# Performance work log

Hardware: AMD Instinct MI355X
Metric: run time of the kernel (lower is better)

## Reference

```python
import jax, jax.numpy as jnp
import numpy as np
import math

B, L, C_IN, D, H, FACTOR = 32, 512, 32, 512, 8, 1
E = D // H
TOP_K = int(FACTOR * math.log(L))  # 6


def setup_inputs() -> dict:
    key = jax.random.key(0)
    ks = jax.random.split(key, 14)
    s = 0.02
    f = lambda k, shp: jax.random.normal(k, shp, jnp.float32) * s
    return {
        "x": jax.random.normal(ks[0], (B, L, C_IN), jnp.float32),
        "conv_w": f(ks[1], (D, C_IN)),  # Conv1d kernel_size=1 == pointwise linear
        "conv_b": f(ks[2], (D,)),
        "wq": f(ks[3], (D, D)), "bq": f(ks[4], (D,)),
        "wk": f(ks[5], (D, D)), "bk": f(ks[6], (D,)),
        "wv": f(ks[7], (D, D)), "bv": f(ks[8], (D,)),
        "wo": f(ks[9], (D, D)), "bo": f(ks[10], (D,)),
        "lin_w": f(ks[11], (1, D)), "lin_b": f(ks[12], (1,)),
    }


def _autocorrelation(q, k, v):
    # q, k, v: [B, L, H, E]; Autoformer AutoCorrelation (inference delay agg)
    qf = jnp.fft.rfft(q.transpose(0, 2, 3, 1), axis=-1)        # [B,H,E,Lf]
    kf = jnp.fft.rfft(k.transpose(0, 2, 3, 1), axis=-1)
    corr = jnp.fft.irfft(qf * jnp.conj(kf), n=L, axis=-1)       # [B,H,E,L]
    vals = v.transpose(0, 2, 3, 1)                              # [B,H,E,L]
    mean_corr = corr.mean(axis=(1, 2))                          # [B,L]
    weights, delay = jax.lax.top_k(mean_corr, TOP_K)            # [B,k]
    w = jax.nn.softmax(weights, axis=-1)                        # [B,k]
    # gather values at (t + delay) mod L  (== doubled-values trick in torch)
    idx = (jnp.arange(L)[None, None, :] + delay[:, :, None]) % L  # [B,k,L]
    patterns = jnp.take_along_axis(
        vals[:, :, :, None, :], idx[:, None, None, :, :], axis=-1)  # [B,H,E,k,L]
    agg = jnp.einsum('bhekl,bk->bhel', patterns, w)             # [B,H,E,L]
    return agg.transpose(0, 3, 1, 2)                            # [B,L,H,E]


def reference(x, conv_w, conv_b, wq, bq, wk, bk, wv, bv, wo, bo, lin_w, lin_b):
    # pointwise conv1d projection: [B,L,C_IN] -> [B,L,D]
    h = x @ conv_w.T + conv_b
    q = (h @ wq.T + bq).reshape(B, L, H, E)
    k = (h @ wk.T + bk).reshape(B, L, H, E)
    v = (h @ wv.T + bv).reshape(B, L, H, E)
    attn_out = _autocorrelation(q, k, v).reshape(B, L, D)
    new_x = attn_out @ wo.T + bo
    out = h + new_x          # residual
    last = out[:, -1:, :]    # x[:, -1:]
    y = last @ lin_w.T + lin_b  # [B,1,1]
    return y
```

## Files before the change

### kernel.cpp

```cpp
#include <hip/hip_runtime.h>
#include <hip/hip_bf16.h>

#define LL 512
#define BB 32
#define DD 512
#define CINN 32
#define TOPK 6
#define BL (BB * LL)

typedef __attribute__((ext_vector_type(8))) short bf16x8;
typedef __attribute__((ext_vector_type(4))) float f32x4;

__device__ inline float bf2f(ushort u) {
    union { uint i; float f; } c; c.i = ((uint)u) << 16; return c.f;
}
__device__ inline ushort f2bf(float f) {
    union { float f; uint i; } c; c.f = f;
    uint i = c.i;
    return (ushort)((i + 0x7FFFu + ((i >> 16) & 1u)) >> 16);
}
__device__ inline void split_bf(float v, ushort& hi, ushort& lo) {
    hi = f2bf(v);
    lo = f2bf(v - bf2f(hi));
}
__device__ inline uint pk2(ushort a, ushort b) { return (uint)a | ((uint)b << 16); }

__device__ inline bf16x8 frag_ld(const ushort* sm, int r, int s) {
    return *(const bf16x8*)(sm + r * 32 + ((s ^ ((r >> 1) & 3)) << 3));
}

__device__ inline void mfma_step(const ushort* sAh, const ushort* sAl,
                                 const ushort* sBh, const ushort* sBl,
                                 f32x4 acc[4][4], int wr, int wc, int fr, int fs) {
    bf16x8 bh[4], blo[4];
    #pragma unroll
    for (int ni = 0; ni < 4; ++ni) {
        bh[ni]  = frag_ld(sBh, wc + ni * 16 + fr, fs);
        blo[ni] = frag_ld(sBl, wc + ni * 16 + fr, fs);
    }
    #pragma unroll
    for (int mi = 0; mi < 4; ++mi) {
        const bf16x8 ah = frag_ld(sAh, wr + mi * 16 + fr, fs);
        const bf16x8 al = frag_ld(sAl, wr + mi * 16 + fr, fs);
        #pragma unroll
        for (int ni = 0; ni < 4; ++ni) {
            acc[mi][ni] = __builtin_amdgcn_mfma_f32_16x16x32_bf16(ah, bh[ni],  acc[mi][ni], 0, 0, 0);
            acc[mi][ni] = __builtin_amdgcn_mfma_f32_16x16x32_bf16(ah, blo[ni], acc[mi][ni], 0, 0, 0);
            acc[mi][ni] = __builtin_amdgcn_mfma_f32_16x16x32_bf16(al, bh[ni],  acc[mi][ni], 0, 0, 0);
        }
    }
}

__global__ __launch_bounds__(256) void prep_m(
    const float* __restrict__ wq, const float* __restrict__ wk,
    const float* __restrict__ cw,
    const float* __restrict__ lin_w, const float* __restrict__ wo,
    float* __restrict__ Mpart, float* __restrict__ upart)
{
    const int tid = threadIdx.x;
    if (blockIdx.x < 64) {
        __shared__ float cws[512][32];
        __shared__ float wqsT[512][9];
        __shared__ float wksT[512][9];
        __shared__ float aqs[8][32];
        __shared__ float aks[8][32];
        for (int i = tid; i < 4096; i += 256) {
            const int d = i >> 3, q = i & 7;
            *(float4*)&cws[d][q * 4] = *(const float4*)(cw + (long)d * 32 + q * 4);
        }
        const int e0 = blockIdx.x * 8;
        for (int i = tid; i < 4096; i += 256) {
            const int e = i >> 9, d = i & 511;
            wqsT[d][e] = wq[(long)(e0 + e) * 512 + d];
            wksT[d][e] = wk[(long)(e0 + e) * 512 + d];
        }
        __syncthreads();
        const int e_loc = tid >> 5, c = tid & 31;
        float aq = 0.f, ak = 0.f;
        #pragma unroll 4
        for (int d = 0; d < 512; ++d) {
            const float cv = cws[d][c];
            aq += wqsT[d][e_loc] * cv;
            ak += wksT[d][e_loc] * cv;
        }
        aqs[e_loc][c] = aq;
        aks[e_loc][c] = ak;
        __syncthreads();
        const int c_ = tid >> 3, cq = tid & 7;
        float m0 = 0.f, m1 = 0.f, m2 = 0.f, m3 = 0.f;
        #pragma unroll
        for (int e = 0; e < 8; ++e) {
            const float a = aqs[e][c_];
            const float4 k4 = *(const float4*)&aks[e][cq * 4];
            m0 += a * k4.x; m1 += a * k4.y; m2 += a * k4.z; m3 += a * k4.w;
        }
        *(float4*)(Mpart + (long)blockIdx.x * 1024 + c_ * 32 + cq * 4) =
            make_float4(m0, m1, m2, m3);
    } else {
        const int j = blockIdx.x - 64;
        const int n0 = j * 64;
        float u0 = 0.f, u1 = 0.f;
        for (int n = 0; n < 64; ++n) {
            const float lw = lin_w[n0 + n];
            u0 += lw * wo[(long)(n0 + n) * 512 + tid];
            u1 += lw * wo[(long)(n0 + n) * 512 + tid + 256];
        }
        upart[j * 512 + tid] = u0;
        upart[j * 512 + tid + 256] = u1;
    }
}

__global__ __launch_bounds__(256, 2) void corr_fused(
    const float* __restrict__ x,
    const float* __restrict__ Mpart, const float* __restrict__ upart,
    const float* __restrict__ wv,
    float* __restrict__ mcpart, float* __restrict__ v2part)
{
    const int tid = threadIdx.x;
    if (blockIdx.x < 512) {
        __shared__ ushort buf[16384];
        __shared__ float Ml[32][36];
        __shared__ float mcloc[LL];
        ushort* bufAh = buf;
        ushort* bufAl = buf + 4096;
        ushort* bufBh = buf + 8192;
        ushort* bufBl = buf + 12288;

        const int xcd = blockIdx.x & 7, s = blockIdx.x >> 3;
        const int b = xcd * 4 + (s >> 4);
        const int tile = s & 15;
        const int tm = tile >> 2, tn = tile & 3;

        {
            float4 ms = make_float4(0.f, 0.f, 0.f, 0.f);
            for (int p = 0; p < 64; ++p) {
                const float4 v = *(const float4*)(Mpart + (long)p * 1024 + tid * 4);
                ms.x += v.x; ms.y += v.y; ms.z += v.z; ms.w += v.w;
            }
            *(float4*)&Ml[tid >> 3][(tid & 7) * 4] = ms;
        }
        mcloc[tid] = 0.f; mcloc[tid + 256] = 0.f;

        const int r = tid >> 1;
        const int pb = (tid & 1) * 2;
        const int swz = (r >> 1) & 3;
        const float* xA = x + ((long)b * LL + tm * 128 + r) * 32;
        const float* xB = x + ((long)b * LL + tn * 128 + r) * 32;
        float xb[32];
        #pragma unroll
        for (int q = 0; q < 8; ++q)
            *(float4*)&xb[q * 4] = *(const float4*)(xB + q * 4);

        __syncthreads();

        #pragma unroll
        for (int pi = 0; pi < 2; ++pi) {
            const int p = pb + pi;
            const int sl = p ^ swz;
            const int uoff = (r * 4 + p) * 8;
            const float4 a0 = *(const float4*)(xA + sl * 8);
            const float4 a1 = *(const float4*)(xA + sl * 8 + 4);
            const float xe[8] = {a0.x, a0.y, a0.z, a0.w, a1.x, a1.y, a1.z, a1.w};
            ushort xh[8], xl[8];
            #pragma unroll
            for (int j = 0; j < 8; ++j) split_bf(xe[j], xh[j], xl[j]);
            *(uint4*)(bufAh + uoff) = make_uint4(pk2(xh[0], xh[1]), pk2(xh[2], xh[3]),
                                                 pk2(xh[4], xh[5]), pk2(xh[6], xh[7]));
            *(uint4*)(bufAl + uoff) = make_uint4(pk2(xl[0], xl[1]), pk2(xl[2], xl[3]),
                                                 pk2(xl[4], xl[5]), pk2(xl[6], xl[7]));
            float uv[8];
            #pragma unroll
            for (int j = 0; j < 8; ++j) {
                const int c = sl * 8 + j;
                float sacc = 0.f;
                #pragma unroll
                for (int q = 0; q < 8; ++q) {
                    const float4 m = *(const float4*)&Ml[c][q * 4];
                    sacc += m.x * xb[q * 4] + m.y * xb[q * 4 + 1]
                          + m.z * xb[q * 4 + 2] + m.w * xb[q * 4 + 3];
                }
                uv[j] = sacc;
            }
            ushort uh[8], ul[8];
            #pragma unroll
            for (int j = 0; j < 8; ++j) split_bf(uv[j], uh[j], ul[j]);
            *(uint4*)(bufBh + uoff) = make_uint4(pk2(uh[0], uh[1]), pk2(uh[2], uh[3]),
                                                 pk2(uh[4], uh[5]), pk2(uh[6], uh[7]));
            *(uint4*)(bufBl + uoff) = make_uint4(pk2(ul[0], ul[1]), pk2(ul[2], ul[3]),
                                                 pk2(ul[4], ul[5]), pk2(ul[6], ul[7]));
        }
        __syncthreads();

        const int wid = tid >> 6, lane = tid & 63;
        const int wr = (wid >> 1) * 64, wc = (wid & 1) * 64;
        const int fr = lane & 15, fs = lane >> 4;
        f32x4 acc[4][4] = {};
        mfma_step(bufAh, bufAl, bufBh, bufBl, acc, wr, wc, fr, fs);

        const int base = wr - wc + 128 * (tm - tn) + fs * 4 - fr;
        #pragma unroll
        for (int k = -3; k <= 3; ++k) {
            #pragma unroll
            for (int rr = 0; rr < 4; ++rr) {
                float sdg = 0.f;
                #pragma unroll
                for (int mi = 0; mi < 4; ++mi) {
                    const int ni = mi - k;
                    if (ni >= 0 && ni < 4) sdg += acc[mi][ni][rr];
                }
                atomicAdd(&mcloc[(base + 16 * k + rr) & (LL - 1)], sdg);
            }
        }
        __syncthreads();
        float* out = mcpart + ((long)b * 16 + tile) * LL;
        out[tid] = mcloc[tid];
        out[tid + 256] = mcloc[tid + 256];
    } else {
        const int j = blockIdx.x - 512;
        __shared__ float us[64];
        if (tid < 64) {
            float s = 0.f;
            #pragma unroll
            for (int i = 0; i < 8; ++i) s += upart[i * 512 + j * 64 + tid];
            us[tid] = s;
        }
        __syncthreads();
        float s0 = 0.f, s1 = 0.f;
        for (int dl = 0; dl < 64; ++dl) {
            const float ud = us[dl];
            s0 += ud * wv[(long)(j * 64 + dl) * 512 + tid];
            s1 += ud * wv[(long)(j * 64 + dl) * 512 + tid + 256];
        }
        v2part[j * 512 + tid] = s0;
        v2part[j * 512 + tid + 256] = s1;
    }
}

__global__ __launch_bounds__(256) void tail_kernel(
    const float* __restrict__ mcpart, const float* __restrict__ x,
    const float* __restrict__ upart, const float* __restrict__ v2part,
    const float* __restrict__ cw, const float* __restrict__ cb,
    const float* __restrict__ lin_w, const float* __restrict__ bv,
    const float* __restrict__ bo, const float* __restrict__ lin_b,
    float* __restrict__ out)
{
    const int b = blockIdx.x, tid = threadIdx.x;
    const int lane = tid & 63, wid = tid >> 6;
    __shared__ float v2s[512];
    __shared__ float us2[512];
    __shared__ float w3p[8][32];
    __shared__ float w4p[8][32];
    __shared__ float w3s[32];
    __shared__ float w4s[32];
    __shared__ float c2s;
    __shared__ float swv[4];
    __shared__ int   swi[4];
    __shared__ float selv[TOPK];
    __shared__ int   seli[TOPK];
    __shared__ float wts[TOPK];
    __shared__ float redc[4];

    {
        float a0 = 0.f, a1 = 0.f, b0 = 0.f, b1 = 0.f;
        #pragma unroll
        for (int i = 0; i < 8; ++i) {
            a0 += v2part[i * 512 + tid];
            a1 += v2part[i * 512 + tid + 256];
            b0 += upart[i * 512 + tid];
            b1 += upart[i * 512 + tid + 256];
        }
        v2s[tid] = a0; v2s[tid + 256] = a1;
        us2[tid] = b0; us2[tid + 256] = b1;
    }
    __syncthreads();
    {
        const int c = tid & 31, g = tid >> 5;
        float w3 = 0.f, w4 = 0.f;
        for (int dl = 0; dl < 64; ++dl) {
            const int d = g * 64 + dl;
            const float cwv = cw[(long)d * 32 + c];
            w3 += v2s[d] * cwv;
            w4 += lin_w[d] * cwv;
        }
        w3p[g][c] = w3; w4p[g][c] = w4;
    }
    __syncthreads();
    if (tid < 32) {
        float a3 = 0.f, a4 = 0.f;
        #pragma unroll
        for (int g2 = 0; g2 < 8; ++g2) { a3 += w3p[g2][tid]; a4 += w4p[g2][tid]; }
        w3s[tid] = a3; w4s[tid] = a4;
    }
    {
        float p = cb[tid] * (v2s[tid] + lin_w[tid])
                + cb[tid + 256] * (v2s[tid + 256] + lin_w[tid + 256])
                + bv[tid] * us2[tid] + bv[tid + 256] * us2[tid + 256]
                + bo[tid] * lin_w[tid] + bo[tid + 256] * lin_w[tid + 256];
        #pragma unroll
        for (int o = 32; o; o >>= 1) p += __shfl_down(p, o);
        if ((tid & 63) == 0) redc[tid >> 6] = p;
    }
    __syncthreads();
    if (tid == 0) c2s = redc[0] + redc[1] + redc[2] + redc[3] + lin_b[0];

    float v0 = 0.f, v1 = 0.f;
    #pragma unroll
    for (int j = 0; j < 16; ++j) {
        v0 += mcpart[((long)b * 16 + j) * LL + tid];
        v1 += mcpart[((long)b * 16 + j) * LL + tid + 256];
    }
    v0 *= (1.0f / DD); v1 *= (1.0f / DD);

    int live0 = 1, live1 = 1;
    for (int r = 0; r < TOPK; ++r) {
        float bvv = -1e30f; int bi = -1;
        if (live0) { bvv = v0; bi = tid; }
        if (live1 && v1 > bvv) { bvv = v1; bi = tid + 256; }
        #pragma unroll
        for (int o = 32; o; o >>= 1) {
            const float ov = __shfl_down(bvv, o);
            const int oi = __shfl_down(bi, o);
            if (ov > bvv || (ov == bvv && oi < bi)) { bvv = ov; bi = oi; }
        }
        if (lane == 0) { swv[wid] = bvv; swi[wid] = bi; }
        __syncthreads();
        if (tid == 0) {
            float fv = swv[0]; int fi = swi[0];
            #pragma unroll
            for (int w2 = 1; w2 < 4; ++w2) {
                if (swv[w2] > fv || (swv[w2] == fv && swi[w2] < fi)) { fv = swv[w2]; fi = swi[w2]; }
            }
            selv[r] = fv; seli[r] = fi;
        }
        __syncthreads();
        const int w = seli[r];
        if (w == tid)       live0 = 0;
        if (w == tid + 256) live1 = 0;
    }
    if (tid == 0) {
        const float mx = selv[0];
        float e[TOPK], ssum = 0.f;
        #pragma unroll
        for (int k = 0; k < TOPK; ++k) { e[k] = expf(selv[k] - mx); ssum += e[k]; }
        #pragma unroll
        for (int k = 0; k < TOPK; ++k) wts[k] = e[k] / ssum;
    }
    __syncthreads();

    if (tid < CINN) {
        float xm = 0.f;
        #pragma unroll
        for (int k = 0; k < TOPK; ++k) {
            const int r = (LL - 1 + seli[k]) & (LL - 1);
            xm += wts[k] * x[((long)b * LL + r) * CINN + tid];
        }
        const float xlv = x[((long)b * LL + (LL - 1)) * CINN + tid];
        float yv = xlv * w4s[tid] + xm * w3s[tid];
        #pragma unroll
        for (int o = 16; o; o >>= 1) yv += __shfl_down(yv, o);
        if (tid == 0) out[b] = yv + c2s;
    }
}

extern "C" void kernel_launch(void* const* d_in, const int* in_sizes, int n_in,
                              void* d_out, int out_size, void* d_ws, size_t ws_size,
                              hipStream_t stream) {
    const float* x      = (const float*)d_in[0];
    const float* conv_w = (const float*)d_in[1];
    const float* conv_b = (const float*)d_in[2];
    const float* wq     = (const float*)d_in[3];
    const float* wk     = (const float*)d_in[5];
    const float* wv     = (const float*)d_in[7];
    const float* bv     = (const float*)d_in[8];
    const float* wo     = (const float*)d_in[9];
    const float* bo     = (const float*)d_in[10];
    const float* lin_w  = (const float*)d_in[11];
    const float* lin_b  = (const float*)d_in[12];

    char* w = (char*)d_ws;
    float* Mpart  = (float*)w;  w += (long)64 * 1024 * 4;
    float* upart  = (float*)w;  w += (long)8 * 512 * 4;
    float* v2part = (float*)w;  w += (long)8 * 512 * 4;
    float* mcpart = (float*)w;  w += (long)BB * 16 * LL * 4;
    float* yout   = (float*)d_out;

    prep_m<<<72, 256, 0, stream>>>(wq, wk, conv_w, lin_w, wo, Mpart, upart);
    corr_fused<<<520, 256, 0, stream>>>(x, Mpart, upart, wv, mcpart, v2part);
    tail_kernel<<<BB, 256, 0, stream>>>(mcpart, x, upart, v2part,
                                        conv_w, conv_b, lin_w, bv, bo, lin_b, yout);
}
```

Before: 61.75 us.

## Move u/v2 matvecs into single prep block and atomically reduce correlation partials

```diff
diff --git a/kernel.cpp b/kernel.cpp
--- a/kernel.cpp
+++ b/kernel.cpp
@@ -51,11 +51,13 @@
     }
 }
 
-__global__ __launch_bounds__(256) void prep_m(
+__global__ __launch_bounds__(256) void prep_kernel(
     const float* __restrict__ wq, const float* __restrict__ wk,
     const float* __restrict__ cw,
     const float* __restrict__ lin_w, const float* __restrict__ wo,
-    float* __restrict__ Mpart, float* __restrict__ upart)
+    const float* __restrict__ wv,
+    float* __restrict__ Mpart, float* __restrict__ ug,
+    float* __restrict__ v2g, float* __restrict__ mc)
 {
     const int tid = threadIdx.x;
     if (blockIdx.x < 64) {
@@ -64,6 +66,10 @@
         __shared__ float wksT[512][9];
         __shared__ float aqs[8][32];
         __shared__ float aks[8][32];
+        if (blockIdx.x < 32) {
+            mc[blockIdx.x * 512 + tid] = 0.f;
+            mc[blockIdx.x * 512 + tid + 256] = 0.f;
+        }
         for (int i = tid; i < 4096; i += 256) {
             const int d = i >> 3, q = i & 7;
             *(float4*)&cws[d][q * 4] = *(const float4*)(cw + (long)d * 32 + q * 4);
@@ -97,100 +103,105 @@
         *(float4*)(Mpart + (long)blockIdx.x * 1024 + c_ * 32 + cq * 4) =
             make_float4(m0, m1, m2, m3);
     } else {
-        const int j = blockIdx.x - 64;
-        const int n0 = j * 64;
+        __shared__ float us[512];
         float u0 = 0.f, u1 = 0.f;
-        for (int n = 0; n < 64; ++n) {
-            const float lw = lin_w[n0 + n];
-            u0 += lw * wo[(long)(n0 + n) * 512 + tid];
-            u1 += lw * wo[(long)(n0 + n) * 512 + tid + 256];
-        }
-        upart[j * 512 + tid] = u0;
-        upart[j * 512 + tid + 256] = u1;
-    }
-}
-
-__global__ __launch_bounds__(256, 2) void corr_fused(
-    const float* __restrict__ x,
-    const float* __restrict__ Mpart, const float* __restrict__ upart,
-    const float* __restrict__ wv,
-    float* __restrict__ mcpart, float* __restrict__ v2part)
+        for (int n = 0; n < 512; ++n) {
+            const float lw = lin_w[n];
+            u0 += lw * wo[(long)n * 512 + tid];
+            u1 += lw * wo[(long)n * 512 + tid + 256];
+        }
+        us[tid] = u0; us[tid + 256] = u1;
+        ug[tid] = u0; ug[tid + 256] = u1;
+        __syncthreads();
+        float s0 = 0.f, s1 = 0.f;
+        for (int d = 0; d < 512; ++d) {
+            const float ud = us[d];
+            s0 += ud * wv[(long)d * 512 + tid];
+            s1 += ud * wv[(long)d * 512 + tid + 256];
+        }
+        v2g[tid] = s0; v2g[tid + 256] = s1;
+    }
+}
+
+__global__ __launch_bounds__(256, 2) void corr_kernel(
+    const float* __restrict__ x, const float* __restrict__ Mpart,
+    float* __restrict__ mc)
 {
+    __shared__ ushort buf[16384];
+    __shared__ float Ml[32][36];
+    __shared__ float mcloc[LL];
+    ushort* bufAh = buf;
+    ushort* bufAl = buf + 4096;
+    ushort* bufBh = buf + 8192;
+    ushort* bufBl = buf + 12288;
     const int tid = threadIdx.x;
-    if (blockIdx.x < 512) {
-        __shared__ ushort buf[16384];
-        __shared__ float Ml[32][36];
-        __shared__ float mcloc[LL];
-        ushort* bufAh = buf;
-        ushort* bufAl = buf + 4096;
-        ushort* bufBh = buf + 8192;
-        ushort* bufBl = buf + 12288;
-
-        const int xcd = blockIdx.x & 7, s = blockIdx.x >> 3;
-        const int b = xcd * 4 + (s >> 4);
-        const int tile = s & 15;
-        const int tm = tile >> 2, tn = tile & 3;
-
-        {
-            float4 ms = make_float4(0.f, 0.f, 0.f, 0.f);
-            for (int p = 0; p < 64; ++p) {
-                const float4 v = *(const float4*)(Mpart + (long)p * 1024 + tid * 4);
-                ms.x += v.x; ms.y += v.y; ms.z += v.z; ms.w += v.w;
+
+    const int xcd = blockIdx.x & 7, s = blockIdx.x >> 3;
+    const int b = xcd * 4 + (s >> 4);
+    const int tile = s & 15;
+    const int tm = tile >> 2, tn = tile & 3;
+
+    {
+        float4 ms = make_float4(0.f, 0.f, 0.f, 0.f);
+        for (int p = 0; p < 64; ++p) {
+            const float4 v = *(const float4*)(Mpart + (long)p * 1024 + tid * 4);
+            ms.x += v.x; ms.y += v.y; ms.z += v.z; ms.w += v.w;
+        }
+        *(float4*)&Ml[tid >> 3][(tid & 7) * 4] = ms;
+    }
+    mcloc[tid] = 0.f; mcloc[tid + 256] = 0.f;
+
+    const int r = tid >> 1;
+    const int pb = (tid & 1) * 2;
+    const int swz = (r >> 1) & 3;
+    const float* xA = x + ((long)b * LL + tm * 128 + r) * 32;
+    const float* xB = x + ((long)b * LL + tn * 128 + r) * 32;
+    float xb[32];
+    #pragma unroll
+    for (int q = 0; q < 8; ++q)
+        *(float4*)&xb[q * 4] = *(const float4*)(xB + q * 4);
+
+    __syncthreads();
+
+    #pragma unroll
+    for (int pi = 0; pi < 2; ++pi) {
+        const int p = pb + pi;
+        const int sl = p ^ swz;
+        const int uoff = (r * 4 + p) * 8;
+        const float4 a0 = *(const float4*)(xA + sl * 8);
+        const float4 a1 = *(const float4*)(xA + sl * 8 + 4);
+        const float xe[8] = {a0.x, a0.y, a0.z, a0.w, a1.x, a1.y, a1.z, a1.w};
+        ushort xh[8], xl[8];
+        #pragma unroll
+        for (int j = 0; j < 8; ++j) split_bf(xe[j], xh[j], xl[j]);
+        *(uint4*)(bufAh + uoff) = make_uint4(pk2(xh[0], xh[1]), pk2(xh[2], xh[3]),
+                                             pk2(xh[4], xh[5]), pk2(xh[6], xh[7]));
+        *(uint4*)(bufAl + uoff) = make_uint4(pk2(xl[0], xl[1]), pk2(xl[2], xl[3]),
+                                             pk2(xl[4], xl[5]), pk2(xl[6], xl[7]));
+        float uv[8];
+        #pragma unroll
+        for (int j = 0; j < 8; ++j) {
+            const int c = sl * 8 + j;
+            float sacc = 0.f;
+            #pragma unroll
+            for (int q = 0; q < 8; ++q) {
+                const float4 m = *(const float4*)&Ml[c][q * 4];
+                sacc += m.x * xb[q * 4] + m.y * xb[q * 4 + 1]
+                      + m.z * xb[q * 4 + 2] + m.w * xb[q * 4 + 3];
             }
-            *(float4*)&Ml[tid >> 3][(tid & 7) * 4] = ms;
-        }
-        mcloc[tid] = 0.f; mcloc[tid + 256] = 0.f;
-
-        const int r = tid >> 1;
-        const int pb = (tid & 1) * 2;
-        const int swz = (r >> 1) & 3;
-        const float* xA = x + ((long)b * LL + tm * 128 + r) * 32;
-        const float* xB = x + ((long)b * LL + tn * 128 + r) * 32;
-        float xb[32];
-        #pragma unroll
-        for (int q = 0; q < 8; ++q)
-            *(float4*)&xb[q * 4] = *(const float4*)(xB + q * 4);
-
-        __syncthreads();
-
-        #pragma unroll
-        for (int pi = 0; pi < 2; ++pi) {
-            const int p = pb + pi;
-            const int sl = p ^ swz;
-            const int uoff = (r * 4 + p) * 8;
-            const float4 a0 = *(const float4*)(xA + sl * 8);
-            const float4 a1 = *(const float4*)(xA + sl * 8 + 4);
-            const float xe[8] = {a0.x, a0.y, a0.z, a0.w, a1.x, a1.y, a1.z, a1.w};
-            ushort xh[8], xl[8];
-            #pragma unroll
-            for (int j = 0; j < 8; ++j) split_bf(xe[j], xh[j], xl[j]);
-            *(uint4*)(bufAh + uoff) = make_uint4(pk2(xh[0], xh[1]), pk2(xh[2], xh[3]),
-                                                 pk2(xh[4], xh[5]), pk2(xh[6], xh[7]));
-            *(uint4*)(bufAl + uoff) = make_uint4(pk2(xl[0], xl[1]), pk2(xl[2], xl[3]),
-                                                 pk2(xl[4], xl[5]), pk2(xl[6], xl[7]));
-            float uv[8];
-            #pragma unroll
-            for (int j = 0; j < 8; ++j) {
-                const int c = sl * 8 + j;
-                float sacc = 0.f;
-                #pragma unroll
-                for (int q = 0; q < 8; ++q) {
-                    const float4 m = *(const float4*)&Ml[c][q * 4];
-                    sacc += m.x * xb[q * 4] + m.y * xb[q * 4 + 1]
-                          + m.z * xb[q * 4 + 2] + m.w * xb[q * 4 + 3];
-                }
-                uv[j] = sacc;
-            }
-            ushort uh[8], ul[8];
-            #pragma unroll
-            for (int j = 0; j < 8; ++j) split_bf(uv[j], uh[j], ul[j]);
-            *(uint4*)(bufBh + uoff) = make_uint4(pk2(uh[0], uh[1]), pk2(uh[2], uh[3]),
-                                                 pk2(uh[4], uh[5]), pk2(uh[6], uh[7]));
-            *(uint4*)(bufBl + uoff) = make_uint4(pk2(ul[0], ul[1]), pk2(ul[2], ul[3]),
-                                                 pk2(ul[4], ul[5]), pk2(ul[6], ul[7]));
-        }
-        __syncthreads();
-
+            uv[j] = sacc;
+        }
+        ushort uh[8], ul[8];
+        #pragma unroll
+        for (int j = 0; j < 8; ++j) split_bf(uv[j], uh[j], ul[j]);
+        *(uint4*)(bufBh + uoff) = make_uint4(pk2(uh[0], uh[1]), pk2(uh[2], uh[3]),
+                                             pk2(uh[4], uh[5]), pk2(uh[6], uh[7]));
+        *(uint4*)(bufBl + uoff) = make_uint4(pk2(ul[0], ul[1]), pk2(ul[2], ul[3]),
+                                             pk2(ul[4], ul[5]), pk2(ul[6], ul[7]));
+    }
+    __syncthreads();
+
+    {
         const int wid = tid >> 6, lane = tid & 63;
         const int wr = (wid >> 1) * 64, wc = (wid & 1) * 64;
         const int fr = lane & 15, fs = lane >> 4;
@@ -211,34 +222,15 @@
                 atomicAdd(&mcloc[(base + 16 * k + rr) & (LL - 1)], sdg);
             }
         }
-        __syncthreads();
-        float* out = mcpart + ((long)b * 16 + tile) * LL;
-        out[tid] = mcloc[tid];
-        out[tid + 256] = mcloc[tid + 256];
-    } else {
-        const int j = blockIdx.x - 512;
-        __shared__ float us[64];
-        if (tid < 64) {
-            float s = 0.f;
-            #pragma unroll
-            for (int i = 0; i < 8; ++i) s += upart[i * 512 + j * 64 + tid];
-            us[tid] = s;
-        }
-        __syncthreads();
-        float s0 = 0.f, s1 = 0.f;
-        for (int dl = 0; dl < 64; ++dl) {
-            const float ud = us[dl];
-            s0 += ud * wv[(long)(j * 64 + dl) * 512 + tid];
-            s1 += ud * wv[(long)(j * 64 + dl) * 512 + tid + 256];
-        }
-        v2part[j * 512 + tid] = s0;
-        v2part[j * 512 + tid + 256] = s1;
-    }
+    }
+    __syncthreads();
+    atomicAdd(&mc[b * 512 + tid], mcloc[tid]);
+    atomicAdd(&mc[b * 512 + tid + 256], mcloc[tid + 256]);
 }
 
 __global__ __launch_bounds__(256) void tail_kernel(
-    const float* __restrict__ mcpart, const float* __restrict__ x,
-    const float* __restrict__ upart, const float* __restrict__ v2part,
+    const float* __restrict__ mc, const float* __restrict__ x,
+    const float* __restrict__ ug, const float* __restrict__ v2g,
     const float* __restrict__ cw, const float* __restrict__ cb,
     const float* __restrict__ lin_w, const float* __restrict__ bv,
     const float* __restrict__ bo, const float* __restrict__ lin_b,
@@ -260,18 +252,8 @@
     __shared__ float wts[TOPK];
     __shared__ float redc[4];
 
-    {
-        float a0 = 0.f, a1 = 0.f, b0 = 0.f, b1 = 0.f;
-        #pragma unroll
-        for (int i = 0; i < 8; ++i) {
-            a0 += v2part[i * 512 + tid];
-            a1 += v2part[i * 512 + tid + 256];
-            b0 += upart[i * 512 + tid];
-            b1 += upart[i * 512 + tid + 256];
-        }
-        v2s[tid] = a0; v2s[tid + 256] = a1;
-        us2[tid] = b0; us2[tid + 256] = b1;
-    }
+    v2s[tid] = v2g[tid]; v2s[tid + 256] = v2g[tid + 256];
+    us2[tid] = ug[tid];  us2[tid + 256] = ug[tid + 256];
     __syncthreads();
     {
         const int c = tid & 31, g = tid >> 5;
@@ -303,13 +285,8 @@
     __syncthreads();
     if (tid == 0) c2s = redc[0] + redc[1] + redc[2] + redc[3] + lin_b[0];
 
-    float v0 = 0.f, v1 = 0.f;
-    #pragma unroll
-    for (int j = 0; j < 16; ++j) {
-        v0 += mcpart[((long)b * 16 + j) * LL + tid];
-        v1 += mcpart[((long)b * 16 + j) * LL + tid + 256];
-    }
-    v0 *= (1.0f / DD); v1 *= (1.0f / DD);
+    float v0 = mc[b * 512 + tid] * (1.0f / DD);
+    float v1 = mc[b * 512 + tid + 256] * (1.0f / DD);
 
     int live0 = 1, live1 = 1;
     for (int r = 0; r < TOPK; ++r) {
@@ -378,14 +355,15 @@
     const float* lin_b  = (const float*)d_in[12];
 
     char* w = (char*)d_ws;
-    float* Mpart  = (float*)w;  w += (long)64 * 1024 * 4;
-    float* upart  = (float*)w;  w += (long)8 * 512 * 4;
-    float* v2part = (float*)w;  w += (long)8 * 512 * 4;
-    float* mcpart = (float*)w;  w += (long)BB * 16 * LL * 4;
-    float* yout   = (float*)d_out;
-
-    prep_m<<<72, 256, 0, stream>>>(wq, wk, conv_w, lin_w, wo, Mpart, upart);
-    corr_fused<<<520, 256, 0, stream>>>(x, Mpart, upart, wv, mcpart, v2part);
-    tail_kernel<<<BB, 256, 0, stream>>>(mcpart, x, upart, v2part,
+    float* Mpart = (float*)w;  w += (long)64 * 1024 * 4;
+    float* ug    = (float*)w;  w += 512 * 4;
+    float* v2g   = (float*)w;  w += 512 * 4;
+    float* mc    = (float*)w;  w += (long)BB * 512 * 4;
+    float* yout  = (float*)d_out;
+
+    prep_kernel<<<65, 256, 0, stream>>>(wq, wk, conv_w, lin_w, wo, wv,
+                                        Mpart, ug, v2g, mc);
+    corr_kernel<<<512, 256, 0, stream>>>(x, Mpart, mc);
+    tail_kernel<<<BB, 256, 0, stream>>>(mc, x, ug, v2g,
                                         conv_w, conv_b, lin_w, bv, bo, lin_b, yout);
 }
```

Measured after the change: 70.11 us. 1.14x slower.
